# Optimization experiments

Hardware: AMD Instinct MI355X
Metric: run time of the kernel (lower is better)

## Reference

```python
import jax, jax.numpy as jnp
import numpy as np

H = 32          # hidden_dim (forced by targetLayer = Linear(4*32, 1))
IN = 1          # input_size per step
T = 129         # seq_len
S = 4           # 4 parallel LSTM streams: [main, f1, f2, f3]


def setup_inputs() -> dict:
    key = jax.random.key(0)
    ks = jax.random.split(key, 16)
    sc = 1.0 / np.sqrt(H)
    u = lambda k, shape: jax.random.uniform(k, shape, jnp.float32, -sc, sc)
    inp = {
        "x": jax.random.normal(ks[0], (S, T, IN), jnp.float32),
        # layer 0 (input -> hidden), stacked over the 4 LSTMs; gate order i,f,g,o
        "Wih0": u(ks[1], (S, 4 * H, IN)),
        "Whh0": u(ks[2], (S, 4 * H, H)),
        "bih0": u(ks[3], (S, 4 * H)),
        "bhh0": u(ks[4], (S, 4 * H)),
        # layer 1 (hidden -> hidden)
        "Wih1": u(ks[5], (S, 4 * H, H)),
        "Whh1": u(ks[6], (S, 4 * H, H)),
        "bih1": u(ks[7], (S, 4 * H)),
        "bhh1": u(ks[8], (S, 4 * H)),
        # output heads
        "Wt": u(ks[9], (1, 4 * H)),
        "bt": u(ks[10], (1,)),
        "Wf1": u(ks[11], (1, H)),
        "bf1": u(ks[12], (1,)),
        "Wf2": u(ks[13], (1, H)),
        "bf2": u(ks[14], (1,)),
    }
    return inp


def _cell(xin, h, c, Wih, Whh, bih, bhh):
    # xin: [S, in], h/c: [S, H]; fused 4-stream LSTM cell, PyTorch gate order i,f,g,o
    g = jnp.einsum('sgi,si->sg', Wih, xin) + jnp.einsum('sgh,sh->sg', Whh, h) + bih + bhh
    i, f, gg, o = jnp.split(g, 4, axis=-1)
    c2 = jax.nn.sigmoid(f) * c + jax.nn.sigmoid(i) * jnp.tanh(gg)
    h2 = jax.nn.sigmoid(o) * jnp.tanh(c2)
    return h2, c2


def reference(x, Wih0, Whh0, bih0, bhh0, Wih1, Whh1, bih1, bhh1, Wt, bt, Wf1, bf1, Wf2, bf2):
    z = jnp.zeros((S, H), x.dtype)

    def step(carry, xt):
        h0, c0, h1, c1 = carry
        h0, c0 = _cell(xt, h0, c0, Wih0, Whh0, bih0, bhh0)
        h1, c1 = _cell(h0, h1, c1, Wih1, Whh1, bih1, bhh1)
        return (h0, c0, h1, c1), None

    xs = jnp.transpose(x, (1, 0, 2))  # [T, S, IN]
    (h0, c0, h1, c1), _ = jax.lax.scan(step, (z, z, z, z), xs)
    hlast = h1  # [S, H], last-step top-layer output; order: main, f1, f2, f3

    targetIn = hlast.reshape(1, S * H)          # torch.cat(...).view(-1, 4H)
    targetOut = targetIn @ Wt.T + bt            # [1, 1]
    f1Out = (hlast[1:2] @ Wf1.T + bf1).reshape(1, 1, 1)
    f2Out = (hlast[2:3] @ Wf2.T + bf2).reshape(1, 1, 1)
    f3Out = (hlast[3:4] @ Wf2.T + bf2).reshape(1, 1, 1)  # original bug: reuses featureLayer2
    return (targetOut, f1Out, f2Out, f3Out)
```

## Files before the change

kernel.cpp:

```cpp
#include <hip/hip_runtime.h>


#define HDIM 32
#define SEQT 129
#define NS 4

__device__ __forceinline__ float rdlane(float v, int k) {
  return __int_as_float(__builtin_amdgcn_readlane(__float_as_int(v), k));
}
__device__ __forceinline__ float fsig(float x) {
  return 1.0f / (1.0f + __expf(-x));
}

__global__ __launch_bounds__(256, 1)
void lstm4_kernel(const float* __restrict__ x,
                  const float* __restrict__ Wih0, const float* __restrict__ Whh0,
                  const float* __restrict__ bih0, const float* __restrict__ bhh0,
                  const float* __restrict__ Wih1, const float* __restrict__ Whh1,
                  const float* __restrict__ bih1, const float* __restrict__ bhh1,
                  const float* __restrict__ Wt,  const float* __restrict__ bt,
                  const float* __restrict__ Wf1, const float* __restrict__ bf1,
                  const float* __restrict__ Wf2, const float* __restrict__ bf2,
                  float* __restrict__ out) {
  const int tid = threadIdx.x;
  const int s = tid >> 6;
  const int l = tid & 63;

  __shared__ float xs[NS * SEQT];
  __shared__ float hfin[NS * HDIM];

  for (int i = tid; i < NS * SEQT; i += 256) xs[i] = x[i];
  __syncthreads();

  const int r1 = s * 128 + l;
  const int r2 = s * 128 + l + 64;

  float wh0a[HDIM], wh0b[HDIM], wi1a[HDIM], wi1b[HDIM], wh1a[HDIM], wh1b[HDIM];
  #pragma unroll
  for (int k = 0; k < HDIM; k += 4) {
    float4 v;
    v = *(const float4*)(Whh0 + r1 * 32 + k);
    wh0a[k] = v.x; wh0a[k+1] = v.y; wh0a[k+2] = v.z; wh0a[k+3] = v.w;
    v = *(const float4*)(Whh0 + r2 * 32 + k);
    wh0b[k] = v.x; wh0b[k+1] = v.y; wh0b[k+2] = v.z; wh0b[k+3] = v.w;
    v = *(const float4*)(Wih1 + r1 * 32 + k);
    wi1a[k] = v.x; wi1a[k+1] = v.y; wi1a[k+2] = v.z; wi1a[k+3] = v.w;
    v = *(const float4*)(Wih1 + r2 * 32 + k);
    wi1b[k] = v.x; wi1b[k+1] = v.y; wi1b[k+2] = v.z; wi1b[k+3] = v.w;
    v = *(const float4*)(Whh1 + r1 * 32 + k);
    wh1a[k] = v.x; wh1a[k+1] = v.y; wh1a[k+2] = v.z; wh1a[k+3] = v.w;
    v = *(const float4*)(Whh1 + r2 * 32 + k);
    wh1b[k] = v.x; wh1b[k+1] = v.y; wh1b[k+2] = v.z; wh1b[k+3] = v.w;
  }
  const float wx0a = Wih0[r1];
  const float wx0b = Wih0[r2];
  const float b0a  = bih0[r1] + bhh0[r1];
  const float b0b  = bih0[r2] + bhh0[r2];
  const float b1a  = bih1[r1] + bhh1[r1];
  const float b1b  = bih1[r2] + bhh1[r2];

  const bool  lo   = (l < 32);
  const float m2   = lo ? 2.0f : 1.0f;
  const float add2 = lo ? -1.0f : 0.0f;

  float h0s[HDIM], h1s[HDIM];
  #pragma unroll
  for (int k = 0; k < HDIM; ++k) { h0s[k] = 0.0f; h1s[k] = 0.0f; }
  float c0 = 0.0f, c1 = 0.0f;
  float h1new = 0.0f;

  #pragma unroll 1
  for (int t = 0; t < SEQT; ++t) {
    const float xt = xs[s * SEQT + t];

    float p1a = b0a, p1b = 0.f, p1c = 0.f, p1d = 0.f;
    float p2a = b0b, p2b = 0.f, p2c = 0.f, p2d = 0.f;
    p1a = fmaf(wx0a, xt, p1a);
    p2a = fmaf(wx0b, xt, p2a);
    #pragma unroll
    for (int k = 0; k < HDIM; k += 4) {
      p1a = fmaf(wh0a[k],   h0s[k],   p1a);
      p1b = fmaf(wh0a[k+1], h0s[k+1], p1b);
      p1c = fmaf(wh0a[k+2], h0s[k+2], p1c);
      p1d = fmaf(wh0a[k+3], h0s[k+3], p1d);
      p2a = fmaf(wh0b[k],   h0s[k],   p2a);
      p2b = fmaf(wh0b[k+1], h0s[k+1], p2b);
      p2c = fmaf(wh0b[k+2], h0s[k+2], p2c);
      p2d = fmaf(wh0b[k+3], h0s[k+3], p2d);
    }
    const float v1 = (p1a + p1b) + (p1c + p1d);
    const float v2 = (p2a + p2b) + (p2c + p2d);

    const float a1  = fsig(v1);
    const float sv2 = fsig(v2 * m2);
    const float a2  = fmaf(sv2, m2, add2);
    const float p   = a1 * a2;
    const float swf = __shfl_xor(a1, 32);
    const float swo = __shfl_xor(a2, 32);
    c0 = fmaf(swf, c0, p);
    const float th0 = fmaf(fsig(2.0f * c0), 2.0f, -1.0f);
    const float h0new = swo * th0;

    #pragma unroll
    for (int k = 0; k < HDIM; ++k) h0s[k] = rdlane(h0new, k);

    float q1a = b1a, q1b = 0.f, q1c = 0.f, q1d = 0.f;
    float q2a = b1b, q2b = 0.f, q2c = 0.f, q2d = 0.f;
    #pragma unroll
    for (int k = 0; k < HDIM; k += 4) {
      q1a = fmaf(wi1a[k],   h0s[k],   q1a);
      q1b = fmaf(wi1a[k+1], h0s[k+1], q1b);
      q1c = fmaf(wi1a[k+2], h0s[k+2], q1c);
      q1d = fmaf(wi1a[k+3], h0s[k+3], q1d);
      q2a = fmaf(wi1b[k],   h0s[k],   q2a);
      q2b = fmaf(wi1b[k+1], h0s[k+1], q2b);
      q2c = fmaf(wi1b[k+2], h0s[k+2], q2c);
      q2d = fmaf(wi1b[k+3], h0s[k+3], q2d);
      q1a = fmaf(wh1a[k],   h1s[k],   q1a);
      q1b = fmaf(wh1a[k+1], h1s[k+1], q1b);
      q1c = fmaf(wh1a[k+2], h1s[k+2], q1c);
      q1d = fmaf(wh1a[k+3], h1s[k+3], q1d);
      q2a = fmaf(wh1b[k],   h1s[k],   q2a);
      q2b = fmaf(wh1b[k+1], h1s[k+1], q2b);
      q2c = fmaf(wh1b[k+2], h1s[k+2], q2c);
      q2d = fmaf(wh1b[k+3], h1s[k+3], q2d);
    }
    const float w1 = (q1a + q1b) + (q1c + q1d);
    const float w2 = (q2a + q2b) + (q2c + q2d);

    const float A1  = fsig(w1);
    const float sw2 = fsig(w2 * m2);
    const float A2  = fmaf(sw2, m2, add2);
    const float P   = A1 * A2;
    const float SWF = __shfl_xor(A1, 32);
    const float SWO = __shfl_xor(A2, 32);
    c1 = fmaf(SWF, c1, P);
    const float th1 = fmaf(fsig(2.0f * c1), 2.0f, -1.0f);
    h1new = SWO * th1;

    #pragma unroll
    for (int k = 0; k < HDIM; ++k) h1s[k] = rdlane(h1new, k);
  }

  if (l < HDIM) hfin[s * HDIM + l] = h1new;
  __syncthreads();

  float acc = 0.0f;
  if (s == 0) {
    acc = fmaf(Wt[l], hfin[l], Wt[l + 64] * hfin[l + 64]);
  } else {
    const float* Wf = (s == 1) ? Wf1 : Wf2;
    if (l < HDIM) acc = Wf[l] * hfin[s * HDIM + l];
  }
  #pragma unroll
  for (int off = 32; off > 0; off >>= 1) acc += __shfl_xor(acc, off);
  if (l == 0) {
    const float bias = (s == 0) ? bt[0] : ((s == 1) ? bf1[0] : bf2[0]);
    out[s] = acc + bias;
  }
}

extern "C" void kernel_launch(void* const* d_in, const int* in_sizes, int n_in,
                              void* d_out, int out_size, void* d_ws, size_t ws_size,
                              hipStream_t stream) {
  const float* x    = (const float*)d_in[0];
  const float* Wih0 = (const float*)d_in[1];
  const float* Whh0 = (const float*)d_in[2];
  const float* bih0 = (const float*)d_in[3];
  const float* bhh0 = (const float*)d_in[4];
  const float* Wih1 = (const float*)d_in[5];
  const float* Whh1 = (const float*)d_in[6];
  const float* bih1 = (const float*)d_in[7];
  const float* bhh1 = (const float*)d_in[8];
  const float* Wt   = (const float*)d_in[9];
  const float* bt   = (const float*)d_in[10];
  const float* Wf1  = (const float*)d_in[11];
  const float* bf1  = (const float*)d_in[12];
  const float* Wf2  = (const float*)d_in[13];
  const float* bf2  = (const float*)d_in[14];
  float* out = (float*)d_out;

  lstm4_kernel<<<1, 256, 0, stream>>>(x, Wih0, Whh0, bih0, bhh0,
                                      Wih1, Whh1, bih1, bhh1,
                                      Wt, bt, Wf1, bf1, Wf2, bf2, out);
}
```

Measured before the change: 178.7 us.

## Use permlane32 swap, reorder layer-1 matvec, prefetch x, pin weights in VGPRs

Replaces the ds_bpermute-based __shfl_xor(...,32) with the gfx950 v_permlane32_swap instruction, so the gate exchange between lane halves stays in registers instead of going through LDS. Reorders the layer-1 matvec so the Whh1·h1 part, which depends only on the previous step, runs before the Wih1·h0 part and can start before the fresh h0 broadcast is ready. Prefetches the next x value one step ahead, and uses empty asm constraints to keep the weight arrays in VGPRs. Together these shorten the serial per-step critical path, at the risk of relying on an architecture-specific builtin and on register pressure staying manageable.

```diff
diff --git a/kernel.cpp b/kernel.cpp
--- a/kernel.cpp
+++ b/kernel.cpp
@@ -11,6 +11,12 @@
 __device__ __forceinline__ float fsig(float x) {
   return 1.0f / (1.0f + __expf(-x));
 }
+__device__ __forceinline__ float swap_hi(float v) {
+  auto r = __builtin_amdgcn_permlane32_swap(__float_as_int(v), __float_as_int(v),
+                                            false, false);
+  return __int_as_float(r[1]);
+}
+#define PINF(w) asm volatile("" : "+v"(w))
 
 __global__ __launch_bounds__(256, 1)
 void lstm4_kernel(const float* __restrict__ x,
@@ -26,10 +32,11 @@
   const int s = tid >> 6;
   const int l = tid & 63;
 
-  __shared__ float xs[NS * SEQT];
+  __shared__ float xs[NS * SEQT + 1];
   __shared__ float hfin[NS * HDIM];
 
   for (int i = tid; i < NS * SEQT; i += 256) xs[i] = x[i];
+  if (tid == 0) xs[NS * SEQT] = 0.0f;
   __syncthreads();
 
   const int r1 = s * 128 + l;
@@ -37,20 +44,26 @@
 
   float wh0a[HDIM], wh0b[HDIM], wi1a[HDIM], wi1b[HDIM], wh1a[HDIM], wh1b[HDIM];
   #pragma unroll
-  for (int k = 0; k < HDIM; k += 4) {
+  for (int j = 0; j < 8; ++j) {
     float4 v;
-    v = *(const float4*)(Whh0 + r1 * 32 + k);
-    wh0a[k] = v.x; wh0a[k+1] = v.y; wh0a[k+2] = v.z; wh0a[k+3] = v.w;
-    v = *(const float4*)(Whh0 + r2 * 32 + k);
-    wh0b[k] = v.x; wh0b[k+1] = v.y; wh0b[k+2] = v.z; wh0b[k+3] = v.w;
-    v = *(const float4*)(Wih1 + r1 * 32 + k);
-    wi1a[k] = v.x; wi1a[k+1] = v.y; wi1a[k+2] = v.z; wi1a[k+3] = v.w;
-    v = *(const float4*)(Wih1 + r2 * 32 + k);
-    wi1b[k] = v.x; wi1b[k+1] = v.y; wi1b[k+2] = v.z; wi1b[k+3] = v.w;
-    v = *(const float4*)(Whh1 + r1 * 32 + k);
-    wh1a[k] = v.x; wh1a[k+1] = v.y; wh1a[k+2] = v.z; wh1a[k+3] = v.w;
-    v = *(const float4*)(Whh1 + r2 * 32 + k);
-    wh1b[k] = v.x; wh1b[k+1] = v.y; wh1b[k+2] = v.z; wh1b[k+3] = v.w;
+    v = *(const float4*)(Whh0 + r1 * 32 + 4 * j);
+    wh0a[4*j] = v.x; wh0a[4*j+1] = v.y; wh0a[4*j+2] = v.z; wh0a[4*j+3] = v.w;
+    v = *(const float4*)(Whh0 + r2 * 32 + 4 * j);
+    wh0b[4*j] = v.x; wh0b[4*j+1] = v.y; wh0b[4*j+2] = v.z; wh0b[4*j+3] = v.w;
+    v = *(const float4*)(Wih1 + r1 * 32 + 4 * j);
+    wi1a[4*j] = v.x; wi1a[4*j+1] = v.y; wi1a[4*j+2] = v.z; wi1a[4*j+3] = v.w;
+    v = *(const float4*)(Wih1 + r2 * 32 + 4 * j);
+    wi1b[4*j] = v.x; wi1b[4*j+1] = v.y; wi1b[4*j+2] = v.z; wi1b[4*j+3] = v.w;
+    v = *(const float4*)(Whh1 + r1 * 32 + 4 * j);
+    wh1a[4*j] = v.x; wh1a[4*j+1] = v.y; wh1a[4*j+2] = v.z; wh1a[4*j+3] = v.w;
+    v = *(const float4*)(Whh1 + r2 * 32 + 4 * j);
+    wh1b[4*j] = v.x; wh1b[4*j+1] = v.y; wh1b[4*j+2] = v.z; wh1b[4*j+3] = v.w;
+  }
+  #pragma unroll
+  for (int k = 0; k < HDIM; ++k) {
+    PINF(wh0a[k]); PINF(wh0b[k]);
+    PINF(wi1a[k]); PINF(wi1b[k]);
+    PINF(wh1a[k]); PINF(wh1b[k]);
   }
   const float wx0a = Wih0[r1];
   const float wx0b = Wih0[r2];
@@ -69,24 +82,26 @@
   float c0 = 0.0f, c1 = 0.0f;
   float h1new = 0.0f;
 
+  float xt = xs[s * SEQT];
+
   #pragma unroll 1
   for (int t = 0; t < SEQT; ++t) {
-    const float xt = xs[s * SEQT + t];
+    const float xt_next = xs[s * SEQT + t + 1];
 
     float p1a = b0a, p1b = 0.f, p1c = 0.f, p1d = 0.f;
     float p2a = b0b, p2b = 0.f, p2c = 0.f, p2d = 0.f;
     p1a = fmaf(wx0a, xt, p1a);
     p2a = fmaf(wx0b, xt, p2a);
     #pragma unroll
-    for (int k = 0; k < HDIM; k += 4) {
-      p1a = fmaf(wh0a[k],   h0s[k],   p1a);
-      p1b = fmaf(wh0a[k+1], h0s[k+1], p1b);
-      p1c = fmaf(wh0a[k+2], h0s[k+2], p1c);
-      p1d = fmaf(wh0a[k+3], h0s[k+3], p1d);
-      p2a = fmaf(wh0b[k],   h0s[k],   p2a);
-      p2b = fmaf(wh0b[k+1], h0s[k+1], p2b);
-      p2c = fmaf(wh0b[k+2], h0s[k+2], p2c);
-      p2d = fmaf(wh0b[k+3], h0s[k+3], p2d);
+    for (int j = 0; j < 8; ++j) {
+      p1a = fmaf(wh0a[4*j+0], h0s[4*j+0], p1a);
+      p1b = fmaf(wh0a[4*j+1], h0s[4*j+1], p1b);
+      p1c = fmaf(wh0a[4*j+2], h0s[4*j+2], p1c);
+      p1d = fmaf(wh0a[4*j+3], h0s[4*j+3], p1d);
+      p2a = fmaf(wh0b[4*j+0], h0s[4*j+0], p2a);
+      p2b = fmaf(wh0b[4*j+1], h0s[4*j+1], p2b);
+      p2c = fmaf(wh0b[4*j+2], h0s[4*j+2], p2c);
+      p2d = fmaf(wh0b[4*j+3], h0s[4*j+3], p2d);
     }
     const float v1 = (p1a + p1b) + (p1c + p1d);
     const float v2 = (p2a + p2b) + (p2c + p2d);
@@ -95,8 +110,8 @@
     const float sv2 = fsig(v2 * m2);
     const float a2  = fmaf(sv2, m2, add2);
     const float p   = a1 * a2;
-    const float swf = __shfl_xor(a1, 32);
-    const float swo = __shfl_xor(a2, 32);
+    const float swf = swap_hi(a1);
+    const float swo = swap_hi(a2);
     c0 = fmaf(swf, c0, p);
     const float th0 = fmaf(fsig(2.0f * c0), 2.0f, -1.0f);
     const float h0new = swo * th0;
@@ -107,23 +122,26 @@
     float q1a = b1a, q1b = 0.f, q1c = 0.f, q1d = 0.f;
     float q2a = b1b, q2b = 0.f, q2c = 0.f, q2d = 0.f;
     #pragma unroll
-    for (int k = 0; k < HDIM; k += 4) {
-      q1a = fmaf(wi1a[k],   h0s[k],   q1a);
-      q1b = fmaf(wi1a[k+1], h0s[k+1], q1b);
-      q1c = fmaf(wi1a[k+2], h0s[k+2], q1c);
-      q1d = fmaf(wi1a[k+3], h0s[k+3], q1d);
-      q2a = fmaf(wi1b[k],   h0s[k],   q2a);
-      q2b = fmaf(wi1b[k+1], h0s[k+1], q2b);
-      q2c = fmaf(wi1b[k+2], h0s[k+2], q2c);
-      q2d = fmaf(wi1b[k+3], h0s[k+3], q2d);
-      q1a = fmaf(wh1a[k],   h1s[k],   q1a);
-      q1b = fmaf(wh1a[k+1], h1s[k+1], q1b);
-      q1c = fmaf(wh1a[k+2], h1s[k+2], q1c);
-      q1d = fmaf(wh1a[k+3], h1s[k+3], q1d);
-      q2a = fmaf(wh1b[k],   h1s[k],   q2a);
-      q2b = fmaf(wh1b[k+1], h1s[k+1], q2b);
-      q2c = fmaf(wh1b[k+2], h1s[k+2], q2c);
-      q2d = fmaf(wh1b[k+3], h1s[k+3], q2d);
+    for (int j = 0; j < 8; ++j) {
+      q1a = fmaf(wh1a[4*j+0], h1s[4*j+0], q1a);
+      q1b = fmaf(wh1a[4*j+1], h1s[4*j+1], q1b);
+      q1c = fmaf(wh1a[4*j+2], h1s[4*j+2], q1c);
+      q1d = fmaf(wh1a[4*j+3], h1s[4*j+3], q1d);
+      q2a = fmaf(wh1b[4*j+0], h1s[4*j+0], q2a);
+      q2b = fmaf(wh1b[4*j+1], h1s[4*j+1], q2b);
+      q2c = fmaf(wh1b[4*j+2], h1s[4*j+2], q2c);
+      q2d = fmaf(wh1b[4*j+3], h1s[4*j+3], q2d);
+    }
+    #pragma unroll
+    for (int j = 0; j < 8; ++j) {
+      q1a = fmaf(wi1a[4*j+0], h0s[4*j+0], q1a);
+      q1b = fmaf(wi1a[4*j+1], h0s[4*j+1], q1b);
+      q1c = fmaf(wi1a[4*j+2], h0s[4*j+2], q1c);
+      q1d = fmaf(wi1a[4*j+3], h0s[4*j+3], q1d);
+      q2a = fmaf(wi1b[4*j+0], h0s[4*j+0], q2a);
+      q2b = fmaf(wi1b[4*j+1], h0s[4*j+1], q2b);
+      q2c = fmaf(wi1b[4*j+2], h0s[4*j+2], q2c);
+      q2d = fmaf(wi1b[4*j+3], h0s[4*j+3], q2d);
     }
     const float w1 = (q1a + q1b) + (q1c + q1d);
     const float w2 = (q2a + q2b) + (q2c + q2d);
@@ -132,14 +150,16 @@
     const float sw2 = fsig(w2 * m2);
     const float A2  = fmaf(sw2, m2, add2);
     const float P   = A1 * A2;
-    const float SWF = __shfl_xor(A1, 32);
-    const float SWO = __shfl_xor(A2, 32);
+    const float SWF = swap_hi(A1);
+    const float SWO = swap_hi(A2);
     c1 = fmaf(SWF, c1, P);
     const float th1 = fmaf(fsig(2.0f * c1), 2.0f, -1.0f);
     h1new = SWO * th1;
 
     #pragma unroll
     for (int k = 0; k < HDIM; ++k) h1s[k] = rdlane(h1new, k);
+
+    xt = xt_next;
   }
 
   if (l < HDIM) hfin[s * HDIM + l] = h1new;
```

Result: no change. 176.2 us (-1.4%).
